# Kernel optimization log

Measured on AMD Instinct MI355X. Metric: run time of the kernel, lower is better.

The kernel has to match this reference:

```python
import jax, jax.numpy as jnp
import numpy as np

NUM_NODES = 100000
EMBED_DIM = 128
HIDDEN = 128
NUM_EDGES = 1600000


def gcn_conv(x, W, b, src, dst, num_nodes):
    """PyG GCNConv: x' = D^{-1/2} (A+I) D^{-1/2} (x W) + b, symmetric norm with self-loops."""
    x = x @ W  # [N, out]
    loops = jnp.arange(num_nodes, dtype=src.dtype)
    s = jnp.concatenate([src, loops])  # sources incl. self-loops
    d = jnp.concatenate([dst, loops])  # targets incl. self-loops
    deg = jax.ops.segment_sum(jnp.ones_like(d, dtype=x.dtype), d, num_segments=num_nodes)
    dis = jnp.where(deg > 0, jax.lax.rsqrt(deg), 0.0)  # deg^{-1/2}, 0 where isolated
    norm = dis[s] * dis[d]  # [E+N]
    msg = x[s] * norm[:, None]  # gather + scale
    out = jax.ops.segment_sum(msg, d, num_segments=num_nodes)  # scatter-add
    return out + b


def setup_inputs() -> dict:
    key = jax.random.key(0)
    k1, k2, k3, k4, k5, k6 = jax.random.split(key, 6)
    edge_index = jax.random.randint(k1, (2, NUM_EDGES), 0, NUM_NODES, dtype=jnp.int64)
    edge_attr = jax.random.normal(k2, (NUM_EDGES,), dtype=jnp.float32)
    emb = jax.random.normal(k3, (NUM_NODES, EMBED_DIM), dtype=jnp.float32) * 0.1
    W1 = jax.random.normal(k4, (EMBED_DIM, HIDDEN), dtype=jnp.float32) * (1.0 / np.sqrt(EMBED_DIM))
    b1 = jnp.zeros((HIDDEN,), dtype=jnp.float32)
    W2 = jax.random.normal(k5, (HIDDEN, HIDDEN), dtype=jnp.float32) * (1.0 / np.sqrt(HIDDEN))
    b2 = jnp.zeros((HIDDEN,), dtype=jnp.float32)
    return {"edge_index": edge_index, "edge_attr": edge_attr, "emb": emb,
            "W1": W1, "b1": b1, "W2": W2, "b2": b2}


def reference(edge_index, edge_attr, emb, W1, b1, W2, b2):
    src, dst = edge_index[0], edge_index[1]
    x = gcn_conv(emb, W1, b1, src, dst, NUM_NODES)
    x = jax.nn.relu(x)
    x = gcn_conv(x, W2, b2, src, dst, NUM_NODES)
    return x
```

## Files before the change

kernel.cpp:

```cpp
#include <hip/hip_runtime.h>

#define EMB 128
#define NBUC 1024
#define NPART 256

typedef __attribute__((ext_vector_type(8))) short short8;
typedef __attribute__((ext_vector_type(4))) float f32x4;

__device__ __forceinline__ unsigned short f2bf(float f) {
    union { float f; unsigned int i; } v; v.f = f;
    unsigned int x = v.i;
    x += 0x7fffu + ((x >> 16) & 1u);
    return (unsigned short)(x >> 16);
}
__device__ __forceinline__ void acc_bf4(uint2 v, float& a0, float& a1, float& a2, float& a3) {
    union { unsigned int i; float f; } t;
    t.i = v.x << 16;          a0 += t.f;
    t.i = v.x & 0xffff0000u;  a1 += t.f;
    t.i = v.y << 16;          a2 += t.f;
    t.i = v.y & 0xffff0000u;  a3 += t.f;
}


__global__ __launch_bounds__(256) void p1_hist(const int* __restrict__ dst,
                                               int* __restrict__ BH, int E, int chunk) {
    __shared__ int h[NBUC];
    for (int i = threadIdx.x; i < NBUC; i += 256) h[i] = 0;
    __syncthreads();
    int s = blockIdx.x * chunk;
    int e = min(E, s + chunk);
    for (int i = s + threadIdx.x; i < e; i += 256)
        atomicAdd(&h[dst[i] >> 7], 1);
    __syncthreads();
    for (int i = threadIdx.x; i < NBUC; i += 256)
        BH[blockIdx.x * NBUC + i] = h[i];
}

__global__ __launch_bounds__(256) void p_tot(const int* __restrict__ BH,
                                             int* __restrict__ tot) {
    int b = blockIdx.x * 256 + threadIdx.x;
    int s = 0;
    for (int blk = 0; blk < NPART; ++blk) s += BH[blk * NBUC + b];
    tot[b] = s;
}

__global__ __launch_bounds__(1024) void p_scan(const int* __restrict__ tot,
                                               int* __restrict__ base, int E) {
    __shared__ int a[NBUC];
    int t = threadIdx.x;
    int v0 = tot[t];
    a[t] = v0;
    __syncthreads();
    for (int off = 1; off < NBUC; off <<= 1) {
        int v = (t >= off) ? a[t - off] : 0;
        __syncthreads();
        a[t] += v;
        __syncthreads();
    }
    base[t] = a[t] - v0;
    if (t == NBUC - 1) base[NBUC] = E;
}

__global__ __launch_bounds__(256) void p_offs(int* __restrict__ BH,
                                              const int* __restrict__ base) {
    int b = blockIdx.x * 256 + threadIdx.x;
    int run = base[b];
    for (int blk = 0; blk < NPART; ++blk) {
        int* p = &BH[blk * NBUC + b];
        int v = *p;
        *p = run;
        run += v;
    }
}

__global__ __launch_bounds__(256) void p2_scatter(const int* __restrict__ src,
                                                  const int* __restrict__ dst,
                                                  const int* __restrict__ BH,
                                                  int* __restrict__ part,
                                                  int E, int chunk) {
    __shared__ int cnt[NBUC];
    for (int i = threadIdx.x; i < NBUC; i += 256)
        cnt[i] = BH[blockIdx.x * NBUC + i];
    __syncthreads();
    int s = blockIdx.x * chunk;
    int e = min(E, s + chunk);
    for (int i = s + threadIdx.x; i < e; i += 256) {
        int d = dst[i];
        int pos = atomicAdd(&cnt[d >> 7], 1);
        part[pos] = src[i] | ((d & 127) << 17);
    }
}

__global__ __launch_bounds__(256) void p3_csr(const int* __restrict__ part,
                                              const int* __restrict__ base,
                                              int* __restrict__ R, int* __restrict__ adj,
                                              float* __restrict__ dis, int N, int E) {
    __shared__ int hist[128];
    __shared__ int sc[128];
    __shared__ int cnt[128];
    int b = blockIdx.x;
    int n0 = b * 128;
    int nn = min(128, N - n0);
    int s = base[b], e = base[b + 1];
    int t = threadIdx.x;

    if (t < 128) hist[t] = 0;
    __syncthreads();
    for (int i = s + t; i < e; i += 256)
        atomicAdd(&hist[part[i] >> 17], 1);
    __syncthreads();

    if (t < 128) sc[t] = hist[t];
    __syncthreads();
    for (int off = 1; off < 128; off <<= 1) {
        int v = 0;
        if (t < 128 && t >= off) v = sc[t - off];
        __syncthreads();
        if (t < 128) sc[t] += v;
        __syncthreads();
    }
    if (t < 128) {
        int excl = sc[t] - hist[t];
        cnt[t] = excl;
        if (t < nn) {
            R[n0 + t] = s + excl;
            dis[n0 + t] = rsqrtf((float)hist[t] + 1.0f);
        }
    }
    if (b == 0 && t == 0) R[N] = E;
    __syncthreads();

    for (int i = s + t; i < e; i += 256) {
        int p = part[i];
        int pos = atomicAdd(&cnt[p >> 17], 1);
        adj[s + pos] = p & 0x1FFFF;
    }
}

__global__ __launch_bounds__(256) void k_prep_w(const float* __restrict__ W,
                                                unsigned short* __restrict__ Ws) {
    int idx = blockIdx.x * 256 + threadIdx.x;
    int k = idx >> 7, n = idx & 127;
    int kk = k >> 5, q = (k >> 3) & 3, j = k & 7;
    int ct = n >> 4, nn = n & 15;
    int didx = ((((kk * 8 + ct) * 4 + q) * 16 + nn) << 3) + j;
    Ws[didx] = f2bf(W[idx]);
}

template <bool XBF16>
__global__ __launch_bounds__(256) void k_gemm_mfma(
    const void* Xv, const unsigned short* __restrict__ Wsw,
    const float* __restrict__ dis, unsigned short* Y, int N)
{
    __shared__ __align__(16) unsigned short lds[16384];

    {
        const uint4* srcp = (const uint4*)Wsw;
        uint4* dstp = (uint4*)lds;
        for (int i = threadIdx.x; i < 2048; i += 256) dstp[i] = srcp[i];
    }
    __syncthreads();

    const int wave = threadIdx.x >> 6;
    const int lane = threadIdx.x & 63;
    const int q = lane >> 4, nn = lane & 15;
    const int row0 = blockIdx.x * 64 + wave * 16;
    const int arow = row0 + nn;
    const int arc = arow < N ? arow : N - 1;

    f32x4 acc[8];
#pragma unroll
    for (int ct = 0; ct < 8; ++ct) acc[ct] = (f32x4){0.f, 0.f, 0.f, 0.f};

#pragma unroll
    for (int kk = 0; kk < 4; ++kk) {
        short8 af;
        if (XBF16) {
            af = *(const short8*)((const unsigned short*)Xv + (size_t)arc * EMB + kk * 32 + q * 8);
        } else {
            const float* xp = (const float*)Xv + (size_t)arc * EMB + kk * 32 + q * 8;
            float4 u0 = *(const float4*)xp;
            float4 u1 = *(const float4*)(xp + 4);
            af[0] = (short)f2bf(u0.x); af[1] = (short)f2bf(u0.y);
            af[2] = (short)f2bf(u0.z); af[3] = (short)f2bf(u0.w);
            af[4] = (short)f2bf(u1.x); af[5] = (short)f2bf(u1.y);
            af[6] = (short)f2bf(u1.z); af[7] = (short)f2bf(u1.w);
        }
#pragma unroll
        for (int ct = 0; ct < 8; ++ct) {
            short8 bf = ((const short8*)lds)[(kk * 8 + ct) * 64 + lane];
            acc[ct] = __builtin_amdgcn_mfma_f32_16x16x32_bf16(af, bf, acc[ct], 0, 0, 0);
        }
    }

    __syncthreads();

    float dv[4];
#pragma unroll
    for (int r = 0; r < 4; ++r) {
        int gm = row0 + q * 4 + r;
        dv[r] = dis[gm < N ? gm : N - 1];
    }
#pragma unroll
    for (int ct = 0; ct < 8; ++ct) {
#pragma unroll
        for (int r = 0; r < 4; ++r) {
            int ml = wave * 16 + q * 4 + r;
            lds[ml * 136 + ct * 16 + nn] = f2bf(acc[ct][r] * dv[r]);
        }
    }
    __syncthreads();

    const int rbase = blockIdx.x * 64;
    for (int i = threadIdx.x; i < 1024; i += 256) {
        int row = i >> 4, off = i & 15;
        int grow = rbase + row;
        if (grow < N) {
            uint4 v = *(const uint4*)(lds + row * 136 + off * 8);
            *((uint4*)(Y + (size_t)grow * EMB) + off) = v;
        }
    }
}

template <bool RELU, bool BF16OUT>
__global__ __launch_bounds__(256) void k_gather_finalize(
    const int* __restrict__ R, const int* __restrict__ adj,
    const unsigned short* __restrict__ Y, const float* __restrict__ dis,
    const float* __restrict__ bias, void* __restrict__ Outv, int N)
{
    int t = blockIdx.x * 256 + threadIdx.x;
    int n = t >> 5;
    if (n >= N) return;
    int j = (t & 31) * 4;

    int rs = R[n], re = R[n + 1];

    float a0 = 0.f, a1 = 0.f, a2 = 0.f, a3 = 0.f;
    uint2 sv = *(const uint2*)(Y + (size_t)n * EMB + j);
    acc_bf4(sv, a0, a1, a2, a3);

    int e = rs;
    for (; e + 3 < re; e += 4) {
        int s0 = adj[e], s1 = adj[e + 1], s2 = adj[e + 2], s3 = adj[e + 3];
        uint2 v0 = *(const uint2*)(Y + (size_t)s0 * EMB + j);
        uint2 v1 = *(const uint2*)(Y + (size_t)s1 * EMB + j);
        uint2 v2 = *(const uint2*)(Y + (size_t)s2 * EMB + j);
        uint2 v3 = *(const uint2*)(Y + (size_t)s3 * EMB + j);
        acc_bf4(v0, a0, a1, a2, a3);
        acc_bf4(v1, a0, a1, a2, a3);
        acc_bf4(v2, a0, a1, a2, a3);
        acc_bf4(v3, a0, a1, a2, a3);
    }
    for (; e < re; ++e) {
        uint2 v0 = *(const uint2*)(Y + (size_t)adj[e] * EMB + j);
        acc_bf4(v0, a0, a1, a2, a3);
    }

    float dv = dis[n];
    float4 b = *(const float4*)(bias + j);
    float o0 = dv * a0 + b.x;
    float o1 = dv * a1 + b.y;
    float o2 = dv * a2 + b.z;
    float o3 = dv * a3 + b.w;
    if (RELU) {
        o0 = fmaxf(o0, 0.f); o1 = fmaxf(o1, 0.f);
        o2 = fmaxf(o2, 0.f); o3 = fmaxf(o3, 0.f);
    }
    if (BF16OUT) {
        ushort4 o = { f2bf(o0), f2bf(o1), f2bf(o2), f2bf(o3) };
        *(ushort4*)((unsigned short*)Outv + (size_t)n * EMB + j) = o;
    } else {
        float4 o = { o0, o1, o2, o3 };
        *(float4*)((float*)Outv + (size_t)n * EMB + j) = o;
    }
}

extern "C" void kernel_launch(void* const* d_in, const int* in_sizes, int n_in,
                              void* d_out, int out_size, void* d_ws, size_t ws_size,
                              hipStream_t stream) {
    const int* ei = (const int*)d_in[0];
    const int E = in_sizes[0] / 2;
    const float* emb = (const float*)d_in[2];
    const int N = in_sizes[2] / EMB;
    const float* W1 = (const float*)d_in[3];
    const float* b1 = (const float*)d_in[4];
    const float* W2 = (const float*)d_in[5];
    const float* b2 = (const float*)d_in[6];
    float* out = (float*)d_out;

    const int* src = ei;
    const int* dstp = ei + E;

    char* w = (char*)d_ws;
    auto take = [&](size_t bytes) { char* p = w; w += (bytes + 511) & ~(size_t)511; return p; };
    float* dis  = (float*)take((size_t)N * 4);
    int*   R    = (int*)  take((size_t)(N + 1) * 4);
    int*   base = (int*)  take((size_t)(NBUC + 1) * 4);
    int*   tot  = (int*)  take((size_t)NBUC * 4);
    int*   adj  = (int*)  take((size_t)E * 4);
    unsigned short* W1s = (unsigned short*)take((size_t)EMB * EMB * 2);
    unsigned short* W2s = (unsigned short*)take((size_t)EMB * EMB * 2);
    unsigned short* Hb  = (unsigned short*)take((size_t)N * EMB * 2);
    int*   part = (int*)Hb;
    int*   BH   = (int*)((char*)Hb + (((size_t)E * 4 + 511) & ~(size_t)511));
    unsigned short* Y1b = (unsigned short*)d_out;

    const int NB = (N + 127) / 128;
    const int chunk = (E + NPART - 1) / NPART;
    const int gM = (N + 63) / 64;
    const int gG = (N * 32 + 255) / 256;

    p1_hist   <<<NPART, 256, 0, stream>>>(dstp, BH, E, chunk);
    p_tot     <<<NBUC / 256, 256, 0, stream>>>(BH, tot);
    p_scan    <<<1, NBUC, 0, stream>>>(tot, base, E);
    p_offs    <<<NBUC / 256, 256, 0, stream>>>(BH, base);
    p2_scatter<<<NPART, 256, 0, stream>>>(src, dstp, BH, part, E, chunk);
    p3_csr    <<<NB, 256, 0, stream>>>(part, base, R, adj, dis, N, E);

    k_prep_w<<<64, 256, 0, stream>>>(W1, W1s);
    k_prep_w<<<64, 256, 0, stream>>>(W2, W2s);

    k_gemm_mfma<false><<<gM, 256, 0, stream>>>(emb, W1s, dis, Y1b, N);
    k_gather_finalize<true, true><<<gG, 256, 0, stream>>>(R, adj, Y1b, dis, b1, Hb, N);

    k_gemm_mfma<true><<<gM, 256, 0, stream>>>(Hb, W2s, dis, Hb, N);
    k_gather_finalize<false, false><<<gG, 256, 0, stream>>>(R, adj, Hb, dis, b2, out, N);
}
```

Before: 343.9 us.

## Merge scan/offset/weight-prep kernels, halve partitions, widen gather to 16-byte loads

Folds the bucket total, scan and per-partition offset passes and both weight conversion kernels into one five-block launch, cutting four kernel launches. NPART is halved from 256 to 128, so the histogram and scatter passes run with fewer, larger chunks. The gather-finalize kernel now gives each thread 8 bf16 features through 16-byte loads, so 16 threads cover a node instead of 32. Fewer blocks in the scatter and a single-block scan-plus-offset pass may lower parallelism in those stages, and the wider gather uses more registers per thread.

Result: slower. 355.5 us (+3.3%).

```diff
diff --git a/kernel.cpp b/kernel.cpp
--- a/kernel.cpp
+++ b/kernel.cpp
@@ -2,7 +2,7 @@
 
 #define EMB 128
 #define NBUC 1024
-#define NPART 256
+#define NPART 128
 
 typedef __attribute__((ext_vector_type(8))) short short8;
 typedef __attribute__((ext_vector_type(4))) float f32x4;
@@ -13,12 +13,16 @@
     x += 0x7fffu + ((x >> 16) & 1u);
     return (unsigned short)(x >> 16);
 }
-__device__ __forceinline__ void acc_bf4(uint2 v, float& a0, float& a1, float& a2, float& a3) {
+__device__ __forceinline__ void acc_bf8(uint4 v, float* a) {
     union { unsigned int i; float f; } t;
-    t.i = v.x << 16;          a0 += t.f;
-    t.i = v.x & 0xffff0000u;  a1 += t.f;
-    t.i = v.y << 16;          a2 += t.f;
-    t.i = v.y & 0xffff0000u;  a3 += t.f;
+    t.i = v.x << 16;          a[0] += t.f;
+    t.i = v.x & 0xffff0000u;  a[1] += t.f;
+    t.i = v.y << 16;          a[2] += t.f;
+    t.i = v.y & 0xffff0000u;  a[3] += t.f;
+    t.i = v.z << 16;          a[4] += t.f;
+    t.i = v.z & 0xffff0000u;  a[5] += t.f;
+    t.i = v.w << 16;          a[6] += t.f;
+    t.i = v.w & 0xffff0000u;  a[7] += t.f;
 }
 
 
@@ -36,40 +40,48 @@
         BH[blockIdx.x * NBUC + i] = h[i];
 }
 
-__global__ __launch_bounds__(256) void p_tot(const int* __restrict__ BH,
-                                             int* __restrict__ tot) {
-    int b = blockIdx.x * 256 + threadIdx.x;
-    int s = 0;
-    for (int blk = 0; blk < NPART; ++blk) s += BH[blk * NBUC + b];
-    tot[b] = s;
-}
-
-__global__ __launch_bounds__(1024) void p_scan(const int* __restrict__ tot,
-                                               int* __restrict__ base, int E) {
-    __shared__ int a[NBUC];
-    int t = threadIdx.x;
-    int v0 = tot[t];
-    a[t] = v0;
-    __syncthreads();
-    for (int off = 1; off < NBUC; off <<= 1) {
-        int v = (t >= off) ? a[t - off] : 0;
+__global__ __launch_bounds__(1024) void k_mid(int* __restrict__ BH, int* __restrict__ base,
+                                              const float* __restrict__ W1,
+                                              const float* __restrict__ W2,
+                                              unsigned short* __restrict__ W1s,
+                                              unsigned short* __restrict__ W2s, int E) {
+    if (blockIdx.x == 0) {
+        __shared__ int a[NBUC];
+        int t = threadIdx.x;
+        int v0 = 0;
+        for (int blk = 0; blk < NPART; ++blk) v0 += BH[blk * NBUC + t];
+        a[t] = v0;
         __syncthreads();
-        a[t] += v;
-        __syncthreads();
-    }
-    base[t] = a[t] - v0;
-    if (t == NBUC - 1) base[NBUC] = E;
-}
-
-__global__ __launch_bounds__(256) void p_offs(int* __restrict__ BH,
-                                              const int* __restrict__ base) {
-    int b = blockIdx.x * 256 + threadIdx.x;
-    int run = base[b];
-    for (int blk = 0; blk < NPART; ++blk) {
-        int* p = &BH[blk * NBUC + b];
-        int v = *p;
-        *p = run;
-        run += v;
+        for (int off = 1; off < NBUC; off <<= 1) {
+            int v = (t >= off) ? a[t - off] : 0;
+            __syncthreads();
+            a[t] += v;
+            __syncthreads();
+        }
+        int excl = a[t] - v0;
+        base[t] = excl;
+        if (t == NBUC - 1) base[NBUC] = E;
+        int run = excl;
+        for (int blk = 0; blk < NPART; ++blk) {
+            int* p = &BH[blk * NBUC + t];
+            int v = *p;
+            *p = run;
+            run += v;
+        }
+    } else {
+        int id = (blockIdx.x - 1) * 8192 + threadIdx.x;
+#pragma unroll
+        for (int it = 0; it < 8; ++it, id += 1024) {
+            int wsel = id >> 14;
+            int idx = id & 16383;
+            const float* W = wsel ? W2 : W1;
+            unsigned short* Ws = wsel ? W2s : W1s;
+            int k = idx >> 7, n = idx & 127;
+            int kk = k >> 5, q = (k >> 3) & 3, j = k & 7;
+            int ct = n >> 4, nn = n & 15;
+            int didx = ((((kk * 8 + ct) * 4 + q) * 16 + nn) << 3) + j;
+            Ws[didx] = f2bf(W[idx]);
+        }
     }
 }
 
@@ -137,16 +149,6 @@
     }
 }
 
-__global__ __launch_bounds__(256) void k_prep_w(const float* __restrict__ W,
-                                                unsigned short* __restrict__ Ws) {
-    int idx = blockIdx.x * 256 + threadIdx.x;
-    int k = idx >> 7, n = idx & 127;
-    int kk = k >> 5, q = (k >> 3) & 3, j = k & 7;
-    int ct = n >> 4, nn = n & 15;
-    int didx = ((((kk * 8 + ct) * 4 + q) * 16 + nn) << 3) + j;
-    Ws[didx] = f2bf(W[idx]);
-}
-
 template <bool XBF16>
 __global__ __launch_bounds__(256) void k_gemm_mfma(
     const void* Xv, const unsigned short* __restrict__ Wsw,
@@ -229,49 +231,56 @@
     const float* __restrict__ bias, void* __restrict__ Outv, int N)
 {
     int t = blockIdx.x * 256 + threadIdx.x;
-    int n = t >> 5;
+    int n = t >> 4;
     if (n >= N) return;
-    int j = (t & 31) * 4;
+    int j = (t & 15) * 8;
 
     int rs = R[n], re = R[n + 1];
 
-    float a0 = 0.f, a1 = 0.f, a2 = 0.f, a3 = 0.f;
-    uint2 sv = *(const uint2*)(Y + (size_t)n * EMB + j);
-    acc_bf4(sv, a0, a1, a2, a3);
+    float a[8] = {0.f, 0.f, 0.f, 0.f, 0.f, 0.f, 0.f, 0.f};
+    uint4 sv = *(const uint4*)(Y + (size_t)n * EMB + j);
+    acc_bf8(sv, a);
 
     int e = rs;
     for (; e + 3 < re; e += 4) {
         int s0 = adj[e], s1 = adj[e + 1], s2 = adj[e + 2], s3 = adj[e + 3];
-        uint2 v0 = *(const uint2*)(Y + (size_t)s0 * EMB + j);
-        uint2 v1 = *(const uint2*)(Y + (size_t)s1 * EMB + j);
-        uint2 v2 = *(const uint2*)(Y + (size_t)s2 * EMB + j);
-        uint2 v3 = *(const uint2*)(Y + (size_t)s3 * EMB + j);
-        acc_bf4(v0, a0, a1, a2, a3);
-        acc_bf4(v1, a0, a1, a2, a3);
-        acc_bf4(v2, a0, a1, a2, a3);
-        acc_bf4(v3, a0, a1, a2, a3);
+        uint4 v0 = *(const uint4*)(Y + (size_t)s0 * EMB + j);
+        uint4 v1 = *(const uint4*)(Y + (size_t)s1 * EMB + j);
+        uint4 v2 = *(const uint4*)(Y + (size_t)s2 * EMB + j);
+        uint4 v3 = *(const uint4*)(Y + (size_t)s3 * EMB + j);
+        acc_bf8(v0, a);
+        acc_bf8(v1, a);
+        acc_bf8(v2, a);
+        acc_bf8(v3, a);
     }
     for (; e < re; ++e) {
-        uint2 v0 = *(const uint2*)(Y + (size_t)adj[e] * EMB + j);
-        acc_bf4(v0, a0, a1, a2, a3);
+        uint4 v0 = *(const uint4*)(Y + (size_t)adj[e] * EMB + j);
+        acc_bf8(v0, a);
     }
 
     float dv = dis[n];
-    float4 b = *(const float4*)(bias + j);
-    float o0 = dv * a0 + b.x;
-    float o1 = dv * a1 + b.y;
-    float o2 = dv * a2 + b.z;
-    float o3 = dv * a3 + b.w;
+    float4 b0 = *(const float4*)(bias + j);
+    float4 b1 = *(const float4*)(bias + j + 4);
+    float o[8];
+    o[0] = dv * a[0] + b0.x; o[1] = dv * a[1] + b0.y;
+    o[2] = dv * a[2] + b0.z; o[3] = dv * a[3] + b0.w;
+    o[4] = dv * a[4] + b1.x; o[5] = dv * a[5] + b1.y;
+    o[6] = dv * a[6] + b1.z; o[7] = dv * a[7] + b1.w;
     if (RELU) {
-        o0 = fmaxf(o0, 0.f); o1 = fmaxf(o1, 0.f);
-        o2 = fmaxf(o2, 0.f); o3 = fmaxf(o3, 0.f);
+#pragma unroll
+        for (int i = 0; i < 8; ++i) o[i] = fmaxf(o[i], 0.f);
     }
     if (BF16OUT) {
-        ushort4 o = { f2bf(o0), f2bf(o1), f2bf(o2), f2bf(o3) };
-        *(ushort4*)((unsigned short*)Outv + (size_t)n * EMB + j) = o;
+        uint4 p;
+        p.x = (unsigned int)f2bf(o[0]) | ((unsigned int)f2bf(o[1]) << 16);
+        p.y = (unsigned int)f2bf(o[2]) | ((unsigned int)f2bf(o[3]) << 16);
+        p.z = (unsigned int)f2bf(o[4]) | ((unsigned int)f2bf(o[5]) << 16);
+        p.w = (unsigned int)f2bf(o[6]) | ((unsigned int)f2bf(o[7]) << 16);
+        *(uint4*)((unsigned short*)Outv + (size_t)n * EMB + j) = p;
     } else {
-        float4 o = { o0, o1, o2, o3 };
-        *(float4*)((float*)Outv + (size_t)n * EMB + j) = o;
+        float* op = (float*)Outv + (size_t)n * EMB + j;
+        *(float4*)op = make_float4(o[0], o[1], o[2], o[3]);
+        *(float4*)(op + 4) = make_float4(o[4], o[5], o[6], o[7]);
     }
 }
 
@@ -296,7 +305,6 @@
     float* dis  = (float*)take((size_t)N * 4);
     int*   R    = (int*)  take((size_t)(N + 1) * 4);
     int*   base = (int*)  take((size_t)(NBUC + 1) * 4);
-    int*   tot  = (int*)  take((size_t)NBUC * 4);
     int*   adj  = (int*)  take((size_t)E * 4);
     unsigned short* W1s = (unsigned short*)take((size_t)EMB * EMB * 2);
     unsigned short* W2s = (unsigned short*)take((size_t)EMB * EMB * 2);
@@ -308,18 +316,13 @@
     const int NB = (N + 127) / 128;
     const int chunk = (E + NPART - 1) / NPART;
     const int gM = (N + 63) / 64;
-    const int gG = (N * 32 + 255) / 256;
+    const int gG = (N * 16 + 255) / 256;
 
     p1_hist   <<<NPART, 256, 0, stream>>>(dstp, BH, E, chunk);
-    p_tot     <<<NBUC / 256, 256, 0, stream>>>(BH, tot);
-    p_scan    <<<1, NBUC, 0, stream>>>(tot, base, E);
-    p_offs    <<<NBUC / 256, 256, 0, stream>>>(BH, base);
+    k_mid     <<<5, 1024, 0, stream>>>(BH, base, W1, W2, W1s, W2s, E);
     p2_scatter<<<NPART, 256, 0, stream>>>(src, dstp, BH, part, E, chunk);
     p3_csr    <<<NB, 256, 0, stream>>>(part, base, R, adj, dis, N, E);
 
-    k_prep_w<<<64, 256, 0, stream>>>(W1, W1s);
-    k_prep_w<<<64, 256, 0, stream>>>(W2, W2s);
-
     k_gemm_mfma<false><<<gM, 256, 0, stream>>>(emb, W1s, dis, Y1b, N);
     k_gather_finalize<true, true><<<gG, 256, 0, stream>>>(R, adj, Y1b, dis, b1, Hb, N);
 
```
